# Kernel optimization log

Measured on AMD Instinct MI355X. Metric: run time of the kernel, lower is better.

Reference implementation:

```python
import jax, jax.numpy as jnp
import numpy as np

B, SI, ST, C, H, D = 1, 1024, 256, 3072, 24, 128
MLP = 4 * C
EPS = 1e-6
SCALE = 1.0 / float(np.sqrt(D))


def _ln(x):
    m = jnp.mean(x, -1, keepdims=True)
    v = jnp.var(x, -1, keepdims=True)
    return (x - m) / jnp.sqrt(v + EPS)


def _rms(x, w):
    return x * jax.lax.rsqrt(jnp.mean(x * x, -1, keepdims=True) + EPS) * w


def _mod(x, shift, scale):
    # AdaLN modulation: x * (1 + scale) + shift, scale/shift are [B, C]
    return x * (1.0 + scale[:, None, :]) + shift[:, None, :]


def _rot_half(x):
    xr, xi = x[..., 0::2], x[..., 1::2]
    return jnp.stack([-xi, xr], -1).reshape(x.shape)


def _rope(x, cos, sin):
    # x: [B, S, H, D]; cos/sin: [S, D]
    return x * cos[None, :, None, :] + _rot_half(x) * sin[None, :, None, :]


def _forward(img, txt, vec, fc, fs,
             i_mod_w, i_mod_b, i_qkv_w, i_qkv_b, i_qn, i_kn, i_pw, i_pb, i_f1w, i_f1b, i_f2w, i_f2b,
             t_mod_w, t_mod_b, t_qkv_w, t_qkv_b, t_qn, t_kn, t_pw, t_pb, t_f1w, t_f1b, t_f2w, t_f2b):
    sv = jax.nn.silu(vec)
    i_s1, i_c1, i_g1, i_s2, i_c2, i_g2 = jnp.split(sv @ i_mod_w + i_mod_b, 6, -1)
    t_s1, t_c1, t_g1, t_s2, t_c2, t_g2 = jnp.split(sv @ t_mod_w + t_mod_b, 6, -1)

    # img stream: LN -> modulate -> QKV -> qk RMSNorm -> RoPE
    iqkv = (_mod(_ln(img), i_s1, i_c1) @ i_qkv_w + i_qkv_b).reshape(B, SI, 3, H, D)
    iq = _rope(_rms(iqkv[:, :, 0], i_qn), fc, fs)
    ik = _rope(_rms(iqkv[:, :, 1], i_kn), fc, fs)
    iv = iqkv[:, :, 2]

    # txt stream: no RoPE
    tqkv = (_mod(_ln(txt), t_s1, t_c1) @ t_qkv_w + t_qkv_b).reshape(B, ST, 3, H, D)
    tq = _rms(tqkv[:, :, 0], t_qn)
    tk = _rms(tqkv[:, :, 1], t_kn)
    tv = tqkv[:, :, 2]

    q = jnp.concatenate([iq, tq], 1)
    k = jnp.concatenate([ik, tk], 1)
    v = jnp.concatenate([iv, tv], 1)

    logits = jnp.einsum('bqhd,bkhd->bhqk', q, k) * SCALE
    o = jnp.einsum('bhqk,bkhd->bqhd', jax.nn.softmax(logits, -1), v).reshape(B, SI + ST, C)
    ia, ta = o[:, :SI], o[:, SI:]

    img = img + (ia @ i_pw + i_pb) * i_g1[:, None, :]
    h = jax.nn.gelu(_mod(_ln(img), i_s2, i_c2) @ i_f1w + i_f1b, approximate=True)
    img = img + (h @ i_f2w + i_f2b) * i_g2[:, None, :]

    txt = txt + (ta @ t_pw + t_pb) * t_g1[:, None, :]
    h = jax.nn.gelu(_mod(_ln(txt), t_s2, t_c2) @ t_f1w + t_f1b, approximate=True)
    txt = txt + (h @ t_f2w + t_f2b) * t_g2[:, None, :]
    return img, txt


def setup_inputs() -> dict:
    key = jax.random.key(0)
    ki = iter(jax.random.split(key, 32))

    def w(shape, s=0.02):
        return jax.random.normal(next(ki), shape, jnp.float32) * s

    # RoPE tables shaped (img_seq_len, head_dim), interleaved pair layout
    pos = jnp.arange(SI, dtype=jnp.float32)
    inv = 1.0 / (10000.0 ** (jnp.arange(0, D, 2, dtype=jnp.float32) / D))
    ang = pos[:, None] * inv[None, :]
    inp = dict(
        img=jax.random.normal(next(ki), (B, SI, C), jnp.float32),
        txt=jax.random.normal(next(ki), (B, ST, C), jnp.float32),
        vec=jax.random.normal(next(ki), (B, C), jnp.float32),
        freqs_cos=jnp.repeat(jnp.cos(ang), 2, -1),
        freqs_sin=jnp.repeat(jnp.sin(ang), 2, -1),
    )
    for p in ('i', 't'):
        inp[p + '_mod_w'] = w((C, 6 * C)); inp[p + '_mod_b'] = jnp.zeros((6 * C,), jnp.float32)
        inp[p + '_qkv_w'] = w((C, 3 * C)); inp[p + '_qkv_b'] = jnp.zeros((3 * C,), jnp.float32)
        inp[p + '_qn'] = jnp.ones((D,), jnp.float32); inp[p + '_kn'] = jnp.ones((D,), jnp.float32)
        inp[p + '_pw'] = w((C, C)); inp[p + '_pb'] = jnp.zeros((C,), jnp.float32)
        inp[p + '_f1w'] = w((C, MLP)); inp[p + '_f1b'] = jnp.zeros((MLP,), jnp.float32)
        inp[p + '_f2w'] = w((MLP, C)); inp[p + '_f2b'] = jnp.zeros((C,), jnp.float32)
    return inp


def reference(img, txt, vec, freqs_cos, freqs_sin,
              i_mod_w, i_mod_b, i_qkv_w, i_qkv_b, i_qn, i_kn, i_pw, i_pb, i_f1w, i_f1b, i_f2w, i_f2b,
              t_mod_w, t_mod_b, t_qkv_w, t_qkv_b, t_qn, t_kn, t_pw, t_pb, t_f1w, t_f1b, t_f2w, t_f2b):
    return _forward(img, txt, vec, freqs_cos, freqs_sin,
                    i_mod_w, i_mod_b, i_qkv_w, i_qkv_b, i_qn, i_kn, i_pw, i_pb, i_f1w, i_f1b, i_f2w, i_f2b,
                    t_mod_w, t_mod_b, t_qkv_w, t_qkv_b, t_qn, t_kn, t_pw, t_pb, t_f1w, t_f1b, t_f2w, t_f2b)
```

## Files before the change

kernel.cpp:

```cpp
#include <hip/hip_runtime.h>


#define SI 1024
#define ST 256
#define SS 1280
#define CC 3072
#define NH 24
#define DH 128
#define MLPD 12288
#define EPSF 1e-6f
#define SCALEF 0.08838834764831845f

typedef __attribute__((ext_vector_type(4))) float f32x4;
typedef __attribute__((ext_vector_type(8))) __bf16 bf16x8;
typedef unsigned short u16;
typedef unsigned int u32;

__device__ __forceinline__ u16 f2bf(float x) {
    union { float f; u32 u; } v; v.f = x;
    u32 r = v.u + 0x7FFFu + ((v.u >> 16) & 1u);
    return (u16)(r >> 16);
}
__device__ __forceinline__ float bf2f(u16 x) {
    union { u32 u; float f; } v; v.u = ((u32)x) << 16; return v.f;
}

__device__ __forceinline__ int gsw(int r) {
    return ((r >> 2) & 7) ^ ((r & 3) << 1);
}

__global__ __launch_bounds__(256) void k_modvec(
    const float* __restrict__ vec,
    const float* __restrict__ wi, const float* __restrict__ bi,
    const float* __restrict__ wt, const float* __restrict__ bt,
    float* __restrict__ mi, float* __restrict__ mt)
{
    __shared__ float sv[CC];
    __shared__ float part[7][128];
    int t = threadIdx.x;
    for (int i = t; i < CC; i += 256) {
        float x = vec[i];
        sv[i] = x / (1.f + __expf(-x));
    }
    __syncthreads();
    int gc = blockIdx.x;
    int strm = gc >= 144;
    const float* W  = strm ? wt : wi;
    const float* Bv = strm ? bt : bi;
    float* out      = strm ? mt : mi;
    int c0 = (gc % 144) * 128 + 4 * (t & 31);
    int g  = t >> 5;
    const float* wp  = W + (size_t)(g * 384) * (6 * CC) + c0;
    const float* svp = sv + g * 384;
    f32x4 acc = {0.f, 0.f, 0.f, 0.f};
    for (int r = 0; r < 384; ++r) {
        f32x4 wr = *(const f32x4*)(wp + (size_t)r * (6 * CC));
        float s = svp[r];
        acc.x += wr.x * s; acc.y += wr.y * s; acc.z += wr.z * s; acc.w += wr.w * s;
    }
    int li = t & 31;
    if (g > 0) *(f32x4*)&part[g - 1][li * 4] = acc;
    __syncthreads();
    if (g == 0) {
#pragma unroll
        for (int i = 0; i < 7; ++i) {
            f32x4 p = *(const f32x4*)&part[i][li * 4];
            acc.x += p.x; acc.y += p.y; acc.z += p.z; acc.w += p.w;
        }
        f32x4 bb = *(const f32x4*)(Bv + c0);
        acc.x += bb.x; acc.y += bb.y; acc.z += bb.z; acc.w += bb.w;
        *(f32x4*)(out + c0) = acc;
    }
}

__global__ __launch_bounds__(256) void k_lnmod(
    const float* __restrict__ xi, const float* __restrict__ xt,
    const float* __restrict__ shi, const float* __restrict__ sci,
    const float* __restrict__ sht, const float* __restrict__ sct,
    u16* __restrict__ out)
{
    int r = blockIdx.x;
    bool ts = r >= SI;
    const float* xp = ts ? (xt + (size_t)(r - SI) * CC) : (xi + (size_t)r * CC);
    const float* shift = ts ? sht : shi;
    const float* scale = ts ? sct : sci;
    u16* op = out + (size_t)r * CC;
    int t = threadIdx.x;
    float4 v[3];
    float s = 0.f, q = 0.f;
#pragma unroll
    for (int j = 0; j < 3; ++j) {
        v[j] = *(const float4*)(xp + j * 1024 + t * 4);
        s += v[j].x + v[j].y + v[j].z + v[j].w;
        q += v[j].x * v[j].x + v[j].y * v[j].y + v[j].z * v[j].z + v[j].w * v[j].w;
    }
#pragma unroll
    for (int m = 32; m; m >>= 1) { s += __shfl_xor(s, m); q += __shfl_xor(q, m); }
    __shared__ float red[8];
    int w = t >> 6;
    if ((t & 63) == 0) { red[w] = s; red[4 + w] = q; }
    __syncthreads();
    s = red[0] + red[1] + red[2] + red[3];
    q = red[4] + red[5] + red[6] + red[7];
    float mean = s * (1.f / CC);
    float var  = q * (1.f / CC) - mean * mean;
    float inv  = rsqrtf(var + EPSF);
#pragma unroll
    for (int j = 0; j < 3; ++j) {
        int c0 = j * 1024 + t * 4;
        float4 sh = *(const float4*)(shift + c0);
        float4 sc = *(const float4*)(scale + c0);
        ushort4 o;
        o.x = f2bf((v[j].x - mean) * inv * (1.f + sc.x) + sh.x);
        o.y = f2bf((v[j].y - mean) * inv * (1.f + sc.y) + sh.y);
        o.z = f2bf((v[j].z - mean) * inv * (1.f + sc.z) + sh.z);
        o.w = f2bf((v[j].w - mean) * inv * (1.f + sc.w) + sh.w);
        *(ushort4*)(op + c0) = o;
    }
}

template <int V, int BN>
__global__ __launch_bounds__(512, 2) void k_gemm(
    const u16* __restrict__ A,
    const float* __restrict__ Wi, const float* __restrict__ Wt,
    const float* __restrict__ bi, const float* __restrict__ bt,
    void* __restrict__ outv, int MBI, int N, int K, int lda)
{
    constexpr int BM  = 256;
    constexpr int NWN = (BN == 256) ? 4 : 2;
    constexpr int WM  = (BN == 256) ? 128 : 64;
    constexpr int MI  = WM / 16;
    constexpr int NFB = (BN == 256) ? 8 : 4;

    __shared__ u16 lA[2][BM * 64];
    __shared__ u16 lB[2][BN * 64];
    int t = threadIdx.x;
    int m0 = blockIdx.y * BM;
    int n0 = blockIdx.x * BN;
    bool txts = (blockIdx.y >= (unsigned)MBI);
    const float* W = txts ? Wt : Wi;
    const size_t koff = (size_t)blockIdx.z * K;

    int w = __builtin_amdgcn_readfirstlane(t >> 6);
    int lane = t & 63;
    int wm = (w / NWN) * WM, wn = (w % NWN) * 64;
    int lr = lane & 15, lg = lane >> 4;

    f32x4 acc[MI][4];
#pragma unroll
    for (int i = 0; i < MI; ++i)
#pragma unroll
        for (int j = 0; j < 4; ++j) acc[i][j] = (f32x4){0.f, 0.f, 0.f, 0.f};

    const int bn4 = (BN == 256) ? 4 * (t & 63) : 4 * (t & 31);
    const int bk  = (BN == 256) ? 8 * w : 4 * (t >> 5);
    f32x4 fb[NFB];
    const int NT = K >> 6;

    const float* bptr = W + (koff + bk) * (size_t)N + n0 + bn4;
    const int arow = t >> 3;
    const int acsw = ((t & 7) ^ gsw(arow)) * 8;
    const u16* aptr = A + (size_t)(m0 + arow) * lda + koff + acsw;

    auto LOADB = [&]() {
#pragma unroll
        for (int i = 0; i < NFB; ++i)
            fb[i] = *(const f32x4*)(bptr + (size_t)i * N);
        bptr += (size_t)64 * N;
    };
    auto GLDSA = [&](int buf) {
#pragma unroll
        for (int i = 0; i < 4; ++i) {
            const u16* gp = aptr + (size_t)(i * 64) * lda;
            u16* lp = &lA[buf][(i * 512 + t) * 8];
            __builtin_amdgcn_global_load_lds(
                (const __attribute__((address_space(1))) void*)gp,
                (__attribute__((address_space(3))) void*)lp, 16, 0, 0);
        }
        aptr += 64;
    };
    auto CVTWR = [&](int buf) {
        if constexpr (BN == 256) {
#pragma unroll
            for (int j = 0; j < 4; ++j) {
                int n = bn4 + j;
                union { uint4 q; __bf16 h[8]; } u;
#pragma unroll
                for (int i = 0; i < 8; ++i) u.h[i] = (__bf16)fb[i][j];
                int cp = (bk >> 3) ^ gsw(n);
                *(uint4*)&lB[buf][n * 64 + cp * 8] = u.q;
            }
        } else {
#pragma unroll
            for (int j = 0; j < 4; ++j) {
                int n = bn4 + j;
                union { uint2 q; __bf16 h[4]; } u;
#pragma unroll
                for (int i = 0; i < 4; ++i) u.h[i] = (__bf16)fb[i][j];
                int cp = (bk >> 3) ^ gsw(n);
                *(uint2*)&lB[buf][n * 64 + cp * 8 + (bk & 4)] = u.q;
            }
        }
    };
    auto MFMAP = [&](int buf) {
#pragma unroll
        for (int ks = 0; ks < 2; ++ks) {
            bf16x8 bv[4];
#pragma unroll
            for (int j = 0; j < 4; ++j) {
                int n = wn + j * 16 + lr;
                bv[j] = *(const bf16x8*)&lB[buf][n * 64 + (((ks * 4 + lg) ^ gsw(n)) * 8)];
            }
#pragma unroll
            for (int mh = 0; mh < MI / 4; ++mh) {
                bf16x8 af[4];
#pragma unroll
                for (int i2 = 0; i2 < 4; ++i2) {
                    int m = wm + (mh * 4 + i2) * 16 + lr;
                    af[i2] = *(const bf16x8*)&lA[buf][m * 64 + (((ks * 4 + lg) ^ gsw(m)) * 8)];
                }
                __builtin_amdgcn_s_setprio(1);
#pragma unroll
                for (int i2 = 0; i2 < 4; ++i2)
#pragma unroll
                    for (int j = 0; j < 4; ++j)
                        acc[mh * 4 + i2][j] = __builtin_amdgcn_mfma_f32_16x16x32_bf16(
                            af[i2], bv[j], acc[mh * 4 + i2][j], 0, 0, 0);
                __builtin_amdgcn_s_setprio(0);
            }
        }
    };
    auto VMWN = [&]() {
        if constexpr (BN == 256)
            asm volatile("s_waitcnt vmcnt(8) lgkmcnt(0)" ::: "memory");
        else
            asm volatile("s_waitcnt vmcnt(4) lgkmcnt(0)" ::: "memory");
    };

    LOADB();
    GLDSA(0);
    CVTWR(0);
    if (NT > 1) LOADB();
    VMWN();
    __builtin_amdgcn_s_barrier();
    __builtin_amdgcn_sched_barrier(0);

    int cur = 0;
    for (int kt = 0; kt < NT; ++kt) {
        bool s1 = kt + 1 < NT;
        bool s2 = kt + 2 < NT;
        if (s1) {
            GLDSA(cur ^ 1);
            CVTWR(cur ^ 1);
        }
        if (s2) LOADB();
        MFMAP(cur);
        if (s1) {
            if (s2) { VMWN(); }
            else    { asm volatile("s_waitcnt vmcnt(0) lgkmcnt(0)" ::: "memory"); }
            __builtin_amdgcn_s_barrier();
            __builtin_amdgcn_sched_barrier(0);
        }
        cur ^= 1;
    }

    const float* Bb = txts ? bt : bi;
    int MT = gridDim.y * BM;
#pragma unroll
    for (int i = 0; i < MI; ++i) {
#pragma unroll
        for (int j = 0; j < 4; ++j) {
            int col = n0 + wn + j * 16 + lr;
            float bvv = (V == 3) ? 0.f : Bb[col];
#pragma unroll
            for (int e = 0; e < 4; ++e) {
                int row = m0 + wm + i * 16 + lg * 4 + e;
                float val = acc[i][j][e] + bvv;
                if (V == 0) {
                    ((float*)outv)[(size_t)row * N + col] = val;
                } else if (V == 1) {
                    float g = 0.5f * val * (1.f + tanhf(0.7978845608028654f * (val + 0.044715f * val * val * val)));
                    ((u16*)outv)[(size_t)row * N + col] = f2bf(g);
                } else if (V == 2) {
                    ((u16*)outv)[(size_t)row * N + col] = f2bf(val);
                } else {
                    ((float*)outv)[((size_t)blockIdx.z * MT + row) * N + col] = val;
                }
            }
        }
    }
}

__global__ __launch_bounds__(256) void k_red(
    const float* __restrict__ p,
    const float* __restrict__ bi, const float* __restrict__ bt,
    const float* __restrict__ gi, const float* __restrict__ gt,
    const float* __restrict__ basei, const float* __restrict__ baset,
    float* __restrict__ out)
{
    int idx4 = blockIdx.x * 256 + threadIdx.x;
    size_t idx = (size_t)idx4 * 4;
    const size_t MN = (size_t)SS * CC;
    int r = idx4 / 768;
    int c = (idx4 - r * 768) * 4;
    bool ts = r >= SI;
    float4 v0 = *(const float4*)(p + idx);
    float4 v1 = *(const float4*)(p + MN + idx);
    float4 bb = *(const float4*)((ts ? bt : bi) + c);
    float4 gg = *(const float4*)((ts ? gt : gi) + c);
    const float* bp = ts ? (baset + (size_t)(r - SI) * CC + c) : (basei + (size_t)r * CC + c);
    float4 ba = *(const float4*)bp;
    float4 o;
    o.x = ba.x + (v0.x + v1.x + bb.x) * gg.x;
    o.y = ba.y + (v0.y + v1.y + bb.y) * gg.y;
    o.z = ba.z + (v0.z + v1.z + bb.z) * gg.z;
    o.w = ba.w + (v0.w + v1.w + bb.w) * gg.w;
    *(float4*)(out + idx) = o;
}

__global__ __launch_bounds__(256) void k_redln(
    const float* __restrict__ p,
    const float* __restrict__ bi, const float* __restrict__ bt,
    const float* __restrict__ gi, const float* __restrict__ gt,
    const float* __restrict__ basei, const float* __restrict__ baset,
    const float* __restrict__ shi, const float* __restrict__ sci,
    const float* __restrict__ sht, const float* __restrict__ sct,
    float* __restrict__ out, u16* __restrict__ xm)
{
    int r = blockIdx.x;
    int t = threadIdx.x;
    bool ts = r >= SI;
    const size_t MN = (size_t)SS * CC;
    const float* b  = ts ? bt : bi;
    const float* g  = ts ? gt : gi;
    const float* base = ts ? (baset + (size_t)(r - SI) * CC) : (basei + (size_t)r * CC);
    const float* p0 = p + (size_t)r * CC;
    const float* p1 = p0 + MN;
    float* op = out + (size_t)r * CC;
    u16*   xp = xm + (size_t)r * CC;

    float4 v[3];
    float s = 0.f, q = 0.f;
#pragma unroll
    for (int j = 0; j < 3; ++j) {
        int c0 = j * 1024 + t * 4;
        float4 a0 = *(const float4*)(p0 + c0);
        float4 a1 = *(const float4*)(p1 + c0);
        float4 bb = *(const float4*)(b + c0);
        float4 gg = *(const float4*)(g + c0);
        float4 ba = *(const float4*)(base + c0);
        float4 o;
        o.x = ba.x + (a0.x + a1.x + bb.x) * gg.x;
        o.y = ba.y + (a0.y + a1.y + bb.y) * gg.y;
        o.z = ba.z + (a0.z + a1.z + bb.z) * gg.z;
        o.w = ba.w + (a0.w + a1.w + bb.w) * gg.w;
        *(float4*)(op + c0) = o;
        v[j] = o;
        s += o.x + o.y + o.z + o.w;
        q += o.x * o.x + o.y * o.y + o.z * o.z + o.w * o.w;
    }
#pragma unroll
    for (int m = 32; m; m >>= 1) { s += __shfl_xor(s, m); q += __shfl_xor(q, m); }
    __shared__ float red[8];
    int w = t >> 6;
    if ((t & 63) == 0) { red[w] = s; red[4 + w] = q; }
    __syncthreads();
    s = red[0] + red[1] + red[2] + red[3];
    q = red[4] + red[5] + red[6] + red[7];
    float mean = s * (1.f / CC);
    float var  = q * (1.f / CC) - mean * mean;
    float inv  = rsqrtf(var + EPSF);
    const float* sh = ts ? sht : shi;
    const float* sc = ts ? sct : sci;
#pragma unroll
    for (int j = 0; j < 3; ++j) {
        int c0 = j * 1024 + t * 4;
        float4 shv = *(const float4*)(sh + c0);
        float4 scv = *(const float4*)(sc + c0);
        ushort4 o;
        o.x = f2bf((v[j].x - mean) * inv * (1.f + scv.x) + shv.x);
        o.y = f2bf((v[j].y - mean) * inv * (1.f + scv.y) + shv.y);
        o.z = f2bf((v[j].z - mean) * inv * (1.f + scv.z) + shv.z);
        o.w = f2bf((v[j].w - mean) * inv * (1.f + scv.w) + shv.w);
        *(ushort4*)(xp + c0) = o;
    }
}

__global__ __launch_bounds__(256) void k_pack(
    const u16* __restrict__ qkv,
    const float* __restrict__ iqn, const float* __restrict__ ikn,
    const float* __restrict__ tqn, const float* __restrict__ tkn,
    const float* __restrict__ fc, const float* __restrict__ fs,
    u16* __restrict__ qpk, u16* __restrict__ kpk, u16* __restrict__ vpk)
{
    int wid = blockIdx.x * 4 + (threadIdx.x >> 6);
    int lane = threadIdx.x & 63;
    int s = wid / 72;
    int wh = wid % 72;
    int which = wh / 24;
    int h = wh % 24;
    int d = lane * 2;
    const u16* src = qkv + (size_t)s * 9216 + which * 3072 + h * 128 + d;
    ushort2 xv = *(const ushort2*)src;
    float x0 = bf2f(xv.x), x1 = bf2f(xv.y);
    float y0 = x0, y1 = x1;
    if (which < 2) {
        float ssq = x0 * x0 + x1 * x1;
#pragma unroll
        for (int m = 32; m; m >>= 1) ssq += __shfl_xor(ssq, m);
        float inv = rsqrtf(ssq * (1.f / 128.f) + EPSF);
        bool isimg = (s < SI);
        const float* wv = (which == 0) ? (isimg ? iqn : tqn) : (isimg ? ikn : tkn);
        y0 = x0 * inv * wv[d];
        y1 = x1 * inv * wv[d + 1];
        if (isimg) {
            float c0 = fc[s * 128 + d], c1 = fc[s * 128 + d + 1];
            float s0 = fs[s * 128 + d], s1 = fs[s * 128 + d + 1];
            float r0 = y0 * c0 - y1 * s0;
            float r1 = y1 * c1 + y0 * s1;
            y0 = r0; y1 = r1;
        }
        if (which == 0) { y0 *= SCALEF; y1 *= SCALEF; }
    }
    u16* dst = (which == 0) ? qpk : (which == 1) ? kpk : vpk;
    ushort2 o; o.x = f2bf(y0); o.y = f2bf(y1);
    *(ushort2*)(dst + ((size_t)h * SS + s) * 128 + d) = o;
}

__global__ __launch_bounds__(512, 1) void k_attn(
    const u16* __restrict__ qpk, const u16* __restrict__ kpk,
    const u16* __restrict__ vpk, u16* __restrict__ o)
{
    __shared__ u16 lK[128 * 136];
    __shared__ u16 lV[128 * 136];
    __shared__ u16 lP[128 * 136];
    int h = blockIdx.y;
    int q0 = blockIdx.x * 128;
    int t = threadIdx.x, w = t >> 6, lane = t & 63;
    int lr = lane & 15, lg = lane >> 4;
    const u16* qh = qpk + (size_t)h * SS * 128;
    const u16* kh = kpk + (size_t)h * SS * 128;
    const u16* vh = vpk + (size_t)h * SS * 128;

    bf16x8 aq[4];
#pragma unroll
    for (int kk = 0; kk < 4; ++kk)
        aq[kk] = *(const bf16x8*)(qh + (size_t)(q0 + w * 16 + lr) * 128 + kk * 32 + lg * 8);

    const f32x4 fz = {0.f, 0.f, 0.f, 0.f};
    f32x4 oa[8];
#pragma unroll
    for (int j = 0; j < 8; ++j) oa[j] = fz;
    float mrow[4], lrow[4];
#pragma unroll
    for (int e = 0; e < 4; ++e) { mrow[e] = -1e30f; lrow[e] = 0.f; }

    for (int kt = 0; kt < 10; ++kt) {
        int t0 = kt * 128;
        __syncthreads();
#pragma unroll
        for (int it = 0; it < 4; ++it) {
            int c = it * 512 + t;
            int row = c >> 4, part = c & 15;
            uint4 d4 = *(const uint4*)(kh + (size_t)(t0 + row) * 128 + part * 8);
            *(uint4*)(&lK[row * 136 + part * 8]) = d4;
        }
#pragma unroll
        for (int it = 0; it < 2; ++it) {
            int c = it * 512 + t;
            int pr = c >> 4;
            int tt = pr * 2;
            int k = c & 15;
            int d0 = k * 8;
            uint4 a = *(const uint4*)(vh + (size_t)(t0 + tt) * 128 + d0);
            uint4 b = *(const uint4*)(vh + (size_t)(t0 + tt + 1) * 128 + d0);
            const u16* a16 = (const u16*)&a;
            const u16* b16 = (const u16*)&b;
            int ts = tt ^ ((k & 7) << 3);
#pragma unroll
            for (int j = 0; j < 8; ++j) {
                ushort2 pv; pv.x = a16[j]; pv.y = b16[j];
                *(ushort2*)(&lV[(d0 + j) * 136 + ts]) = pv;
            }
        }
        __syncthreads();
        f32x4 sa[8];
#pragma unroll
        for (int j = 0; j < 8; ++j) sa[j] = fz;
#pragma unroll
        for (int kk = 0; kk < 4; ++kk) {
            bf16x8 bk[8];
#pragma unroll
            for (int ni = 0; ni < 8; ++ni)
                bk[ni] = *(const bf16x8*)(&lK[(ni * 16 + lr) * 136 + kk * 32 + lg * 8]);
            __builtin_amdgcn_s_setprio(1);
#pragma unroll
            for (int ni = 0; ni < 8; ++ni)
                sa[ni] = __builtin_amdgcn_mfma_f32_16x16x32_bf16(aq[kk], bk[ni], sa[ni], 0, 0, 0);
            __builtin_amdgcn_s_setprio(0);
        }
#pragma unroll
        for (int e = 0; e < 4; ++e) {
            float mx = sa[0][e];
#pragma unroll
            for (int ni = 1; ni < 8; ++ni) mx = fmaxf(mx, sa[ni][e]);
#pragma unroll
            for (int msk = 1; msk < 16; msk <<= 1) mx = fmaxf(mx, __shfl_xor(mx, msk));
            float mnew = fmaxf(mrow[e], mx);
            float esc = __expf(mrow[e] - mnew);
            mrow[e] = mnew;
            float rsum = 0.f;
#pragma unroll
            for (int ni = 0; ni < 8; ++ni) {
                float p = __expf(sa[ni][e] - mnew);
                sa[ni][e] = p;
                rsum += p;
            }
#pragma unroll
            for (int msk = 1; msk < 16; msk <<= 1) rsum += __shfl_xor(rsum, msk);
            lrow[e] = lrow[e] * esc + rsum;
#pragma unroll
            for (int nd = 0; nd < 8; ++nd) oa[nd][e] *= esc;
        }
#pragma unroll
        for (int ni = 0; ni < 8; ++ni)
#pragma unroll
            for (int e = 0; e < 4; ++e)
                lP[(w * 16 + lg * 4 + e) * 136 + ni * 16 + lr] = f2bf(sa[ni][e]);
#pragma unroll
        for (int kk = 0; kk < 4; ++kk) {
            bf16x8 pa, vb[8];
            pa = *(const bf16x8*)(&lP[(w * 16 + lr) * 136 + kk * 32 + lg * 8]);
#pragma unroll
            for (int nd = 0; nd < 8; ++nd) {
                int d = nd * 16 + lr;
                int ch = (kk * 4 + lg) ^ ((d >> 3) & 7);
                vb[nd] = *(const bf16x8*)(&lV[d * 136 + ch * 8]);
            }
            __builtin_amdgcn_s_setprio(1);
#pragma unroll
            for (int nd = 0; nd < 8; ++nd)
                oa[nd] = __builtin_amdgcn_mfma_f32_16x16x32_bf16(pa, vb[nd], oa[nd], 0, 0, 0);
            __builtin_amdgcn_s_setprio(0);
        }
    }
#pragma unroll
    for (int nd = 0; nd < 8; ++nd) {
#pragma unroll
        for (int e = 0; e < 4; ++e) {
            int row = q0 + w * 16 + lg * 4 + e;
            int col = h * 128 + nd * 16 + lr;
            o[(size_t)row * CC + col] = f2bf(oa[nd][e] / lrow[e]);
        }
    }
}

extern "C" void kernel_launch(void* const* d_in, const int* in_sizes, int n_in,
                              void* d_out, int out_size, void* d_ws, size_t ws_size,
                              hipStream_t stream)
{
    const float* img  = (const float*)d_in[0];
    const float* txt  = (const float*)d_in[1];
    const float* vec  = (const float*)d_in[2];
    const float* fc   = (const float*)d_in[3];
    const float* fs   = (const float*)d_in[4];
    const float* i_mod_w = (const float*)d_in[5];
    const float* i_mod_b = (const float*)d_in[6];
    const float* i_qkv_w = (const float*)d_in[7];
    const float* i_qkv_b = (const float*)d_in[8];
    const float* i_qn  = (const float*)d_in[9];
    const float* i_kn  = (const float*)d_in[10];
    const float* i_pw  = (const float*)d_in[11];
    const float* i_pb  = (const float*)d_in[12];
    const float* i_f1w = (const float*)d_in[13];
    const float* i_f1b = (const float*)d_in[14];
    const float* i_f2w = (const float*)d_in[15];
    const float* i_f2b = (const float*)d_in[16];
    const float* t_mod_w = (const float*)d_in[17];
    const float* t_mod_b = (const float*)d_in[18];
    const float* t_qkv_w = (const float*)d_in[19];
    const float* t_qkv_b = (const float*)d_in[20];
    const float* t_qn  = (const float*)d_in[21];
    const float* t_kn  = (const float*)d_in[22];
    const float* t_pw  = (const float*)d_in[23];
    const float* t_pb  = (const float*)d_in[24];
    const float* t_f1w = (const float*)d_in[25];
    const float* t_f1b = (const float*)d_in[26];
    const float* t_f2w = (const float*)d_in[27];
    const float* t_f2b = (const float*)d_in[28];

    char* ws = (char*)d_ws;
    float* mod_i = (float*)(ws + 0);
    float* mod_t = (float*)(ws + 73728);
    u16*   xmod  = (u16*)(ws + 147456);
    u16*   qkvb  = (u16*)(ws + 8011776);
    u16*   qpk   = (u16*)(ws + 55197696);
    u16*   kpk   = (u16*)(ws + 63062016);
    u16*   vpk   = (u16*)(ws + 70926336);
    u16*   obuf  = (u16*)(ws + 78790656);
    u16*   hbuf  = (u16*)(ws + 8011776);
    float* pbufP = (float*)(ws + 8011776);
    float* pbufF = (float*)(ws + 39469056);

    float* out_img = (float*)d_out;
    float* out_txt = out_img + (size_t)SI * CC;

    k_modvec<<<288, 256, 0, stream>>>(vec, i_mod_w, i_mod_b, t_mod_w, t_mod_b, mod_i, mod_t);

    k_lnmod<<<SS, 256, 0, stream>>>(img, txt, mod_i + 0, mod_i + 3072,
                                    mod_t + 0, mod_t + 3072, xmod);

    k_gemm<2, 256><<<dim3(36, 5, 1), 512, 0, stream>>>(xmod, i_qkv_w, t_qkv_w, i_qkv_b, t_qkv_b,
                                                       qkvb, 4, 9216, CC, CC);

    k_pack<<<23040, 256, 0, stream>>>(qkvb, i_qn, i_kn, t_qn, t_kn, fc, fs, qpk, kpk, vpk);

    k_attn<<<dim3(10, 24), 512, 0, stream>>>(qpk, kpk, vpk, obuf);

    k_gemm<3, 128><<<dim3(24, 5, 2), 512, 0, stream>>>(obuf, i_pw, t_pw, nullptr, nullptr,
                                                       pbufP, 4, CC, CC / 2, CC);
    k_redln<<<SS, 256, 0, stream>>>(pbufP, i_pb, t_pb, mod_i + 6144, mod_t + 6144,
                                    img, txt,
                                    mod_i + 9216, mod_i + 12288,
                                    mod_t + 9216, mod_t + 12288,
                                    out_img, xmod);

    k_gemm<1, 256><<<dim3(48, 5, 1), 512, 0, stream>>>(xmod, i_f1w, t_f1w, i_f1b, t_f1b,
                                                       hbuf, 4, MLPD, CC, CC);

    k_gemm<3, 128><<<dim3(24, 5, 2), 512, 0, stream>>>(hbuf, i_f2w, t_f2w, nullptr, nullptr,
                                                       pbufF, 4, CC, MLPD / 2, MLPD);
    k_red<<<3840, 256, 0, stream>>>(pbufF, i_f2b, t_f2b, mod_i + 15360, mod_t + 15360,
                                    out_img, out_txt, out_img);
}
```

Measured before the change: 646.1 us.

## Read A fragments directly from global memory in wide-tile GEMMs, skipping LDS staging

Adds a k_gemmA kernel for the QKV and FC1 GEMMs. Each wave loads its bf16 A fragments straight from global memory into registers, so A is no longer staged through LDS with global_load_lds; only the converted B tile goes through shared memory. This halves LDS use and drops the A-side LDS traffic. In exchange, A loads are uncoalesced per-lane 16-byte global reads with no explicit vmcnt wait before the MFMAs, and A rows are reread across the four N-waves through cache. The remaining k_gemm is specialised to BN=128 for the split-K projection GEMMs.

```diff
diff --git a/kernel.cpp b/kernel.cpp
--- a/kernel.cpp
+++ b/kernel.cpp
@@ -119,19 +119,142 @@
     }
 }
 
-template <int V, int BN>
+template <int V>
+__global__ __launch_bounds__(512, 2) void k_gemmA(
+    const u16* __restrict__ A,
+    const float* __restrict__ Wi, const float* __restrict__ Wt,
+    const float* __restrict__ bi, const float* __restrict__ bt,
+    void* __restrict__ outv, int MBI, int N, int K, int lda)
+{
+    __shared__ u16 lB[2][256 * 64];
+    int t = threadIdx.x;
+    int m0 = blockIdx.y * 256;
+    int n0 = blockIdx.x * 256;
+    bool txts = (blockIdx.y >= (unsigned)MBI);
+    const float* W = txts ? Wt : Wi;
+
+    int w = __builtin_amdgcn_readfirstlane(t >> 6);
+    int lane = t & 63;
+    int wm = (w >> 2) * 128, wn = (w & 3) * 64;
+    int lr = lane & 15, lg = lane >> 4;
+
+    f32x4 acc[8][4];
+#pragma unroll
+    for (int i = 0; i < 8; ++i)
+#pragma unroll
+        for (int j = 0; j < 4; ++j) acc[i][j] = (f32x4){0.f, 0.f, 0.f, 0.f};
+
+    const int bn4 = 4 * (t & 63);
+    const int bk  = 8 * w;
+    f32x4 fb[8];
+    const int NT = K >> 6;
+
+    const float* bptr = W + (size_t)bk * N + n0 + bn4;
+    const u16* aptr = A + (size_t)(m0 + wm + lr) * lda + lg * 8;
+
+    auto LOADB = [&]() {
+#pragma unroll
+        for (int i = 0; i < 8; ++i)
+            fb[i] = *(const f32x4*)(bptr + (size_t)i * N);
+        bptr += (size_t)64 * N;
+    };
+    auto CVTWR = [&](int buf) {
+#pragma unroll
+        for (int j = 0; j < 4; ++j) {
+            int n = bn4 + j;
+            union { uint4 q; __bf16 h[8]; } u;
+#pragma unroll
+            for (int i = 0; i < 8; ++i) u.h[i] = (__bf16)fb[i][j];
+            int cp = (bk >> 3) ^ gsw(n);
+            *(uint4*)&lB[buf][n * 64 + cp * 8] = u.q;
+        }
+    };
+    auto MFMAP = [&](int buf) {
+#pragma unroll
+        for (int ks = 0; ks < 2; ++ks) {
+            bf16x8 bv[4];
+#pragma unroll
+            for (int j = 0; j < 4; ++j) {
+                int n = wn + j * 16 + lr;
+                bv[j] = *(const bf16x8*)&lB[buf][n * 64 + (((ks * 4 + lg) ^ gsw(n)) * 8)];
+            }
+            bf16x8 af0[4], af1[4];
+#pragma unroll
+            for (int i2 = 0; i2 < 4; ++i2)
+                af0[i2] = *(const bf16x8*)(aptr + (size_t)(i2 * 16) * lda + ks * 32);
+#pragma unroll
+            for (int i2 = 0; i2 < 4; ++i2)
+                af1[i2] = *(const bf16x8*)(aptr + (size_t)(64 + i2 * 16) * lda + ks * 32);
+            __builtin_amdgcn_s_setprio(1);
+#pragma unroll
+            for (int i2 = 0; i2 < 4; ++i2)
+#pragma unroll
+                for (int j = 0; j < 4; ++j)
+                    acc[i2][j] = __builtin_amdgcn_mfma_f32_16x16x32_bf16(
+                        af0[i2], bv[j], acc[i2][j], 0, 0, 0);
+#pragma unroll
+            for (int i2 = 0; i2 < 4; ++i2)
+#pragma unroll
+                for (int j = 0; j < 4; ++j)
+                    acc[4 + i2][j] = __builtin_amdgcn_mfma_f32_16x16x32_bf16(
+                        af1[i2], bv[j], acc[4 + i2][j], 0, 0, 0);
+            __builtin_amdgcn_s_setprio(0);
+        }
+        aptr += 64;
+    };
+
+    LOADB();
+    CVTWR(0);
+    if (NT > 1) LOADB();
+    asm volatile("s_waitcnt lgkmcnt(0)" ::: "memory");
+    __builtin_amdgcn_s_barrier();
+    __builtin_amdgcn_sched_barrier(0);
+
+    int cur = 0;
+    for (int kt = 0; kt < NT; ++kt) {
+        bool s1 = kt + 1 < NT;
+        bool s2 = kt + 2 < NT;
+        if (s1) CVTWR(cur ^ 1);
+        if (s2) LOADB();
+        MFMAP(cur);
+        if (s1) {
+            asm volatile("s_waitcnt lgkmcnt(0)" ::: "memory");
+            __builtin_amdgcn_s_barrier();
+            __builtin_amdgcn_sched_barrier(0);
+        }
+        cur ^= 1;
+    }
+
+    const float* Bb = txts ? bt : bi;
+#pragma unroll
+    for (int i = 0; i < 8; ++i) {
+#pragma unroll
+        for (int j = 0; j < 4; ++j) {
+            int col = n0 + wn + j * 16 + lr;
+            float bvv = Bb[col];
+#pragma unroll
+            for (int e = 0; e < 4; ++e) {
+                int row = m0 + wm + i * 16 + lg * 4 + e;
+                float val = acc[i][j][e] + bvv;
+                if (V == 1) {
+                    float g = 0.5f * val * (1.f + tanhf(0.7978845608028654f * (val + 0.044715f * val * val * val)));
+                    ((u16*)outv)[(size_t)row * N + col] = f2bf(g);
+                } else {
+                    ((u16*)outv)[(size_t)row * N + col] = f2bf(val);
+                }
+            }
+        }
+    }
+}
+
+template <int V>
 __global__ __launch_bounds__(512, 2) void k_gemm(
     const u16* __restrict__ A,
     const float* __restrict__ Wi, const float* __restrict__ Wt,
     const float* __restrict__ bi, const float* __restrict__ bt,
     void* __restrict__ outv, int MBI, int N, int K, int lda)
 {
-    constexpr int BM  = 256;
-    constexpr int NWN = (BN == 256) ? 4 : 2;
-    constexpr int WM  = (BN == 256) ? 128 : 64;
-    constexpr int MI  = WM / 16;
-    constexpr int NFB = (BN == 256) ? 8 : 4;
-
+    constexpr int BM = 256, BN = 128;
     __shared__ u16 lA[2][BM * 64];
     __shared__ u16 lB[2][BN * 64];
     int t = threadIdx.x;
@@ -143,18 +266,18 @@
 
     int w = __builtin_amdgcn_readfirstlane(t >> 6);
     int lane = t & 63;
-    int wm = (w / NWN) * WM, wn = (w % NWN) * 64;
+    int wm = (w >> 1) * 64, wn = (w & 1) * 64;
     int lr = lane & 15, lg = lane >> 4;
 
-    f32x4 acc[MI][4];
-#pragma unroll
-    for (int i = 0; i < MI; ++i)
+    f32x4 acc[4][4];
+#pragma unroll
+    for (int i = 0; i < 4; ++i)
 #pragma unroll
         for (int j = 0; j < 4; ++j) acc[i][j] = (f32x4){0.f, 0.f, 0.f, 0.f};
 
-    const int bn4 = (BN == 256) ? 4 * (t & 63) : 4 * (t & 31);
-    const int bk  = (BN == 256) ? 8 * w : 4 * (t >> 5);
-    f32x4 fb[NFB];
+    const int bn4 = 4 * (t & 31);
+    const int bk  = 4 * (t >> 5);
+    f32x4 fb[4];
     const int NT = K >> 6;
 
     const float* bptr = W + (koff + bk) * (size_t)N + n0 + bn4;
@@ -164,7 +287,7 @@
 
     auto LOADB = [&]() {
 #pragma unroll
-        for (int i = 0; i < NFB; ++i)
+        for (int i = 0; i < 4; ++i)
             fb[i] = *(const f32x4*)(bptr + (size_t)i * N);
         bptr += (size_t)64 * N;
     };
@@ -180,26 +303,14 @@
         aptr += 64;
     };
     auto CVTWR = [&](int buf) {
-        if constexpr (BN == 256) {
-#pragma unroll
-            for (int j = 0; j < 4; ++j) {
-                int n = bn4 + j;
-                union { uint4 q; __bf16 h[8]; } u;
-#pragma unroll
-                for (int i = 0; i < 8; ++i) u.h[i] = (__bf16)fb[i][j];
-                int cp = (bk >> 3) ^ gsw(n);
-                *(uint4*)&lB[buf][n * 64 + cp * 8] = u.q;
-            }
-        } else {
-#pragma unroll
-            for (int j = 0; j < 4; ++j) {
-                int n = bn4 + j;
-                union { uint2 q; __bf16 h[4]; } u;
-#pragma unroll
-                for (int i = 0; i < 4; ++i) u.h[i] = (__bf16)fb[i][j];
-                int cp = (bk >> 3) ^ gsw(n);
-                *(uint2*)&lB[buf][n * 64 + cp * 8 + (bk & 4)] = u.q;
-            }
+#pragma unroll
+        for (int j = 0; j < 4; ++j) {
+            int n = bn4 + j;
+            union { uint2 q; __bf16 h[4]; } u;
+#pragma unroll
+            for (int i = 0; i < 4; ++i) u.h[i] = (__bf16)fb[i][j];
+            int cp = (bk >> 3) ^ gsw(n);
+            *(uint2*)&lB[buf][n * 64 + cp * 8 + (bk & 4)] = u.q;
         }
     };
     auto MFMAP = [&](int buf) {
@@ -211,37 +322,28 @@
                 int n = wn + j * 16 + lr;
                 bv[j] = *(const bf16x8*)&lB[buf][n * 64 + (((ks * 4 + lg) ^ gsw(n)) * 8)];
             }
-#pragma unroll
-            for (int mh = 0; mh < MI / 4; ++mh) {
-                bf16x8 af[4];
-#pragma unroll
-                for (int i2 = 0; i2 < 4; ++i2) {
-                    int m = wm + (mh * 4 + i2) * 16 + lr;
-                    af[i2] = *(const bf16x8*)&lA[buf][m * 64 + (((ks * 4 + lg) ^ gsw(m)) * 8)];
-                }
-                __builtin_amdgcn_s_setprio(1);
-#pragma unroll
-                for (int i2 = 0; i2 < 4; ++i2)
-#pragma unroll
-                    for (int j = 0; j < 4; ++j)
-                        acc[mh * 4 + i2][j] = __builtin_amdgcn_mfma_f32_16x16x32_bf16(
-                            af[i2], bv[j], acc[mh * 4 + i2][j], 0, 0, 0);
-                __builtin_amdgcn_s_setprio(0);
+            bf16x8 af[4];
+#pragma unroll
+            for (int i2 = 0; i2 < 4; ++i2) {
+                int m = wm + i2 * 16 + lr;
+                af[i2] = *(const bf16x8*)&lA[buf][m * 64 + (((ks * 4 + lg) ^ gsw(m)) * 8)];
             }
-        }
-    };
-    auto VMWN = [&]() {
-        if constexpr (BN == 256)
-            asm volatile("s_waitcnt vmcnt(8) lgkmcnt(0)" ::: "memory");
-        else
-            asm volatile("s_waitcnt vmcnt(4) lgkmcnt(0)" ::: "memory");
+            __builtin_amdgcn_s_setprio(1);
+#pragma unroll
+            for (int i2 = 0; i2 < 4; ++i2)
+#pragma unroll
+                for (int j = 0; j < 4; ++j)
+                    acc[i2][j] = __builtin_amdgcn_mfma_f32_16x16x32_bf16(
+                        af[i2], bv[j], acc[i2][j], 0, 0, 0);
+            __builtin_amdgcn_s_setprio(0);
+        }
     };
 
     LOADB();
     GLDSA(0);
     CVTWR(0);
     if (NT > 1) LOADB();
-    VMWN();
+    asm volatile("s_waitcnt vmcnt(4) lgkmcnt(0)" ::: "memory");
     __builtin_amdgcn_s_barrier();
     __builtin_amdgcn_sched_barrier(0);
 
@@ -256,36 +358,24 @@
         if (s2) LOADB();
         MFMAP(cur);
         if (s1) {
-            if (s2) { VMWN(); }
-            else    { asm volatile("s_waitcnt vmcnt(0) lgkmcnt(0)" ::: "memory"); }
+            if (s2) asm volatile("s_waitcnt vmcnt(4) lgkmcnt(0)" ::: "memory");
+            else    asm volatile("s_waitcnt vmcnt(0) lgkmcnt(0)" ::: "memory");
             __builtin_amdgcn_s_barrier();
             __builtin_amdgcn_sched_barrier(0);
         }
         cur ^= 1;
     }
 
-    const float* Bb = txts ? bt : bi;
     int MT = gridDim.y * BM;
 #pragma unroll
-    for (int i = 0; i < MI; ++i) {
+    for (int i = 0; i < 4; ++i) {
 #pragma unroll
         for (int j = 0; j < 4; ++j) {
             int col = n0 + wn + j * 16 + lr;
-            float bvv = (V == 3) ? 0.f : Bb[col];
 #pragma unroll
             for (int e = 0; e < 4; ++e) {
                 int row = m0 + wm + i * 16 + lg * 4 + e;
-                float val = acc[i][j][e] + bvv;
-                if (V == 0) {
-                    ((float*)outv)[(size_t)row * N + col] = val;
-                } else if (V == 1) {
-                    float g = 0.5f * val * (1.f + tanhf(0.7978845608028654f * (val + 0.044715f * val * val * val)));
-                    ((u16*)outv)[(size_t)row * N + col] = f2bf(g);
-                } else if (V == 2) {
-                    ((u16*)outv)[(size_t)row * N + col] = f2bf(val);
-                } else {
-                    ((float*)outv)[((size_t)blockIdx.z * MT + row) * N + col] = val;
-                }
+                ((float*)outv)[((size_t)blockIdx.z * MT + row) * N + col] = acc[i][j][e];
             }
         }
     }
@@ -610,26 +700,26 @@
     k_lnmod<<<SS, 256, 0, stream>>>(img, txt, mod_i + 0, mod_i + 3072,
                                     mod_t + 0, mod_t + 3072, xmod);
 
-    k_gemm<2, 256><<<dim3(36, 5, 1), 512, 0, stream>>>(xmod, i_qkv_w, t_qkv_w, i_qkv_b, t_qkv_b,
-                                                       qkvb, 4, 9216, CC, CC);
+    k_gemmA<2><<<dim3(36, 5, 1), 512, 0, stream>>>(xmod, i_qkv_w, t_qkv_w, i_qkv_b, t_qkv_b,
+                                                   qkvb, 4, 9216, CC, CC);
 
     k_pack<<<23040, 256, 0, stream>>>(qkvb, i_qn, i_kn, t_qn, t_kn, fc, fs, qpk, kpk, vpk);
 
     k_attn<<<dim3(10, 24), 512, 0, stream>>>(qpk, kpk, vpk, obuf);
 
-    k_gemm<3, 128><<<dim3(24, 5, 2), 512, 0, stream>>>(obuf, i_pw, t_pw, nullptr, nullptr,
-                                                       pbufP, 4, CC, CC / 2, CC);
+    k_gemm<3><<<dim3(24, 5, 2), 512, 0, stream>>>(obuf, i_pw, t_pw, nullptr, nullptr,
+                                                  pbufP, 4, CC, CC / 2, CC);
     k_redln<<<SS, 256, 0, stream>>>(pbufP, i_pb, t_pb, mod_i + 6144, mod_t + 6144,
                                     img, txt,
                                     mod_i + 9216, mod_i + 12288,
                                     mod_t + 9216, mod_t + 12288,
                                     out_img, xmod);
 
-    k_gemm<1, 256><<<dim3(48, 5, 1), 512, 0, stream>>>(xmod, i_f1w, t_f1w, i_f1b, t_f1b,
-                                                       hbuf, 4, MLPD, CC, CC);
-
-    k_gemm<3, 128><<<dim3(24, 5, 2), 512, 0, stream>>>(hbuf, i_f2w, t_f2w, nullptr, nullptr,
-                                                       pbufF, 4, CC, MLPD / 2, MLPD);
+    k_gemmA<1><<<dim3(48, 5, 1), 512, 0, stream>>>(xmod, i_f1w, t_f1w, i_f1b, t_f1b,
+                                                   hbuf, 4, MLPD, CC, CC);
+
+    k_gemm<3><<<dim3(24, 5, 2), 512, 0, stream>>>(hbuf, i_f2w, t_f2w, nullptr, nullptr,
+                                                  pbufF, 4, CC, MLPD / 2, MLPD);
     k_red<<<3840, 256, 0, stream>>>(pbufF, i_f2b, t_f2b, mod_i + 15360, mod_t + 15360,
                                     out_img, out_txt, out_img);
 }
```

After: 936.8 us. +45.0%, slower.
